# Optimization experiments

Hardware: AMD Instinct MI355X
Metric: run time of the kernel (lower is better)

Reference implementation:

```python
import jax, jax.numpy as jnp
import numpy as np

PAD = 50
CLUSTERING_WEIGHT = 1.0
SAMPLE_NUMBER = 8192
EPS = 1e-6


def setup_inputs() -> dict:
    key = jax.random.key(0)
    k1, k2 = jax.random.split(key)
    n, c, h, w = 2, 19, 512, 512
    output = jax.random.uniform(k1, (n, c, h, w), dtype=jnp.float32)
    hw_cropped = (h - 2 * PAD) * (w - 2 * PAD)  # 412*412 = 169744
    sample = jax.random.randint(k2, (SAMPLE_NUMBER,), 0, hw_cropped, dtype=jnp.int64)
    return {"output": output, "sample": sample}


def reference(output, sample):
    n, c, h, w = output.shape
    # crop pad border
    out = output[:, :, PAD:h - PAD, PAD:w - PAD]  # [n, c, h', w']
    prob = out.reshape(n, c, -1)[:, :, sample]     # [n, c, S]
    prob_t = jnp.swapaxes(prob, 1, 2)              # [n, S, c]
    # sampled similarity: [n, S, S] (memory-heavy intermediate)
    sim = jnp.einsum('nsc,ntc->nst', prob_t, prob_t)
    ind = jnp.argmax(sim, axis=2)                  # [n, S]
    # nearest[b, i, k] = prob_t[b, ind[b, i], k]
    nearest = jnp.take_along_axis(prob_t, ind[:, :, None], axis=1)  # [n, S, c]
    # robust_crossentropy(pred=prob_t, tgt=nearest)
    loss = -(nearest * jnp.log(prob_t + EPS))
    loss = loss.mean() * CLUSTERING_WEIGHT
    return loss[None]  # shape [1]
```

## Files before the change

kernel.cpp:

```cpp
#include <hip/hip_runtime.h>
#include <math.h>

#define N 2
#define C 19
#define H 512
#define W 512
#define PADC 50
#define WC 412
#define S 8192
#define CP 20
#define XP 64
#define NCHUNK 16
#define CHUNKT (S / NCHUNK)
#define TTS 128
#define NSTG (CHUNKT / TTS)
#define TPS (TTS / 32)
#define LPITCH 72
#define EPSF 1e-6f

typedef __attribute__((ext_vector_type(8))) short short8;
typedef __attribute__((ext_vector_type(16))) float f32x16;

__device__ __forceinline__ unsigned short f2bf_rne(float x) {
    unsigned u = __float_as_uint(x);
    unsigned r = (u + 0x7FFFu + ((u >> 16) & 1u)) >> 16;
    return (unsigned short)r;
}
__device__ __forceinline__ float bf2f(unsigned short h) {
    return __uint_as_float(((unsigned)h) << 16);
}
__device__ __forceinline__ float max16c(const f32x16 a) {
    float m0 = fmaxf(fmaxf(a[0], a[1]), a[2]);
    float m1 = fmaxf(fmaxf(a[3], a[4]), a[5]);
    float m2 = fmaxf(fmaxf(a[6], a[7]), a[8]);
    float m3 = fmaxf(fmaxf(a[9], a[10]), a[11]);
    float m4 = fmaxf(fmaxf(a[12], a[13]), a[14]);
    float n0 = fmaxf(fmaxf(m0, m1), m2);
    float n1 = fmaxf(fmaxf(m3, m4), a[15]);
    return fmaxf(fmaxf(n0, n1), 0.f);
}

__global__ void gather_k(const float* __restrict__ out4d,
                         const int* __restrict__ sample,
                         float* __restrict__ P32,
                         unsigned short* __restrict__ XA,
                         unsigned short* __restrict__ XB) {
    int idx = blockIdx.x * blockDim.x + threadIdx.x;
    int lane = idx & 63;
    int hi   = lane >> 5;
    int l    = lane & 31;
    int ns = idx >> 5;
    int nn = ns >> 13;
    int s  = ns & (S - 1);
    int smp = sample[s];
    int row = smp / WC;
    int col = smp - row * WC;
    const float* base = out4d + ((size_t)nn * C) * H * W
                      + (size_t)(PADC + row) * W + (PADC + col);
    float v = 0.f;
    if (l < C) v = base[(size_t)l * (H * W)];
    unsigned hb = f2bf_rne(v);
    unsigned lb = f2bf_rne(v - bf2f((unsigned short)hb));

    if (l < CP) P32[(size_t)ns * CP + l] = v;

    int base32 = hi << 5;
    int srcA = base32 + (l < C ? l : l - C);
    int srcB = base32 + (l < C ? l : l - 6);
    unsigned lbA = (unsigned)__shfl((int)lb, srcA, 64);
    unsigned hbA = (unsigned)__shfl((int)hb, srcA, 64);
    unsigned lbB = (unsigned)__shfl((int)lb, srcB, 64);
    unsigned hbB = (unsigned)__shfl((int)hb, srcB, 64);

    unsigned short a0 = (unsigned short)(l < C ? hb : lbA);
    unsigned short a1 = (unsigned short)(l < C ? hb : (l < 25 ? lbB : 0u));
    unsigned short b0 = (unsigned short)hbA;
    unsigned short b1 = (unsigned short)(l < C ? lb : (l < 25 ? hbB : 0u));

    unsigned short* xa = XA + (size_t)ns * XP;
    unsigned short* xb = XB + (size_t)ns * XP;
    xa[l]      = a0;
    xa[32 + l] = a1;
    xb[l]      = b0;
    xb[32 + l] = b1;
}

__global__ __launch_bounds__(512, 4) void argmax_k(const unsigned short* __restrict__ XA,
                                                   const unsigned short* __restrict__ XB,
                                                   unsigned* __restrict__ keys) {
    __shared__ unsigned short lds[2][TTS * LPITCH];
    int b = blockIdx.x;
    int chunk  = b & (NCHUNK - 1);
    int sgroup = (b >> 4) & 15;
    int nn     = b >> 8;
    int tid  = threadIdx.x;
    int w    = tid >> 6;
    int lane = tid & 63;
    int col  = lane & 31;
    int hi   = lane >> 5;
    int s0   = (sgroup * 16 + w) * 32;
    int s1   = s0 + 256;
    int t0   = chunk * CHUNKT;
    const unsigned short* XAn = XA + (size_t)nn * S * XP;
    const unsigned short* XBn = XB + (size_t)nn * S * XP;

    short8 bfA[4], bfB[4];
    {
        const unsigned short* ba = XBn + (size_t)(s0 + col) * XP + hi * 8;
        bfA[0] = *(const short8*)(ba);      bfA[1] = *(const short8*)(ba + 16);
        bfA[2] = *(const short8*)(ba + 32); bfA[3] = *(const short8*)(ba + 48);
        const unsigned short* bb = XBn + (size_t)(s1 + col) * XP + hi * 8;
        bfB[0] = *(const short8*)(bb);      bfB[1] = *(const short8*)(bb + 16);
        bfB[2] = *(const short8*)(bb + 32); bfB[3] = *(const short8*)(bb + 48);
    }

    f32x16 zacc = {};
    unsigned kA = 0u, kB = 0u;

    int r0 = tid >> 3, j0 = tid & 7;
    int r1 = r0 + 64;

    {
        const float4* src = (const float4*)(XAn + (size_t)t0 * XP);
        *(float4*)(&lds[0][r0 * LPITCH + j0 * 8]) = src[tid];
        *(float4*)(&lds[0][r1 * LPITCH + j0 * 8]) = src[tid + 512];
    }
    __syncthreads();

    int cur = 0;
    for (int st = 0; st < NSTG; ++st) {
        float4 na, nb;
        if (st + 1 < NSTG) {
            const float4* srcn = (const float4*)(XAn + (size_t)(t0 + (st + 1) * TTS) * XP);
            na = srcn[tid]; nb = srcn[tid + 512];
        }
        const unsigned short* bs = &lds[cur][0];
        #pragma unroll
        for (int ts = 0; ts < TPS; ++ts) {
            const unsigned short* arow = bs + (ts * 32 + col) * LPITCH + hi * 8;
            short8 a0 = *(const short8*)(arow);
            short8 a1 = *(const short8*)(arow + 16);
            short8 a2 = *(const short8*)(arow + 32);
            short8 a3 = *(const short8*)(arow + 48);
            f32x16 accA = __builtin_amdgcn_mfma_f32_32x32x16_bf16(a0, bfA[0], zacc, 0, 0, 0);
            accA = __builtin_amdgcn_mfma_f32_32x32x16_bf16(a1, bfA[1], accA, 0, 0, 0);
            accA = __builtin_amdgcn_mfma_f32_32x32x16_bf16(a2, bfA[2], accA, 0, 0, 0);
            accA = __builtin_amdgcn_mfma_f32_32x32x16_bf16(a3, bfA[3], accA, 0, 0, 0);
            f32x16 accB = __builtin_amdgcn_mfma_f32_32x32x16_bf16(a0, bfB[0], zacc, 0, 0, 0);
            accB = __builtin_amdgcn_mfma_f32_32x32x16_bf16(a1, bfB[1], accB, 0, 0, 0);
            accB = __builtin_amdgcn_mfma_f32_32x32x16_bf16(a2, bfB[2], accB, 0, 0, 0);
            accB = __builtin_amdgcn_mfma_f32_32x32x16_bf16(a3, bfB[3], accB, 0, 0, 0);
            int tile = st * TPS + ts;
            unsigned tb = (unsigned)(63 - tile);
            unsigned vA = (__float_as_uint(max16c(accA)) & ~63u) | tb;
            unsigned vB = (__float_as_uint(max16c(accB)) & ~63u) | tb;
            kA = kA > vA ? kA : vA;
            kB = kB > vB ? kB : vB;
        }
        if (st + 1 < NSTG) {
            *(float4*)(&lds[cur ^ 1][r0 * LPITCH + j0 * 8]) = na;
            *(float4*)(&lds[cur ^ 1][r1 * LPITCH + j0 * 8]) = nb;
        }
        __syncthreads();
        cur ^= 1;
    }

    unsigned oA = __shfl(kA, lane ^ 32, 64);
    unsigned oB = __shfl(kB, lane ^ 32, 64);
    kA = kA > oA ? kA : oA;
    kB = kB > oB ? kB : oB;
    if (lane < 32) {
        size_t basek = ((size_t)nn * NCHUNK + chunk) * S;
        keys[basek + s0 + col] = kA;
        keys[basek + s1 + col] = kB;
    }
}

__global__ __launch_bounds__(256) void refine_loss_k(const float* __restrict__ P32,
                                                     const unsigned* __restrict__ keys,
                                                     float* __restrict__ bsum) {
    __shared__ float red[8];
    int tid = threadIdx.x;
    int lane = tid & 63;
    int hi = lane >> 5;
    int l  = lane & 31;
    int ns = blockIdx.x * 8 + (tid >> 6) * 2 + hi;
    int nn = ns >> 13;
    int s  = ns & (S - 1);

    const unsigned* kp = keys + (size_t)nn * NCHUNK * S + s;
    unsigned bk = kp[0]; int bc = 0;
    #pragma unroll
    for (int c = 1; c < NCHUNK; ++c) {
        unsigned k = kp[(size_t)c * S];
        if ((k >> 6) > (bk >> 6)) { bk = k; bc = c; }
    }
    int tile = 63 - (int)(bk & 63u);
    int tbase = bc * CHUNKT + tile * 32;

    const float* Pn = P32 + (size_t)nn * S * CP;
    const float* sr = Pn + (size_t)s * CP;
    const float* tr = Pn + (size_t)(tbase + l) * CP;
    float v = 0.f;
    #pragma unroll
    for (int c = 0; c < C; ++c) v = fmaf(sr[c], tr[c], v);
    int t = tbase + l;
    #pragma unroll
    for (int off = 16; off > 0; off >>= 1) {
        float ov = __shfl_xor(v, off, 32);
        int   ot = __shfl_xor(t, off, 32);
        if (ov > v || (ov == v && ot < t)) { v = ov; t = ot; }
    }
    const float* nrow = Pn + (size_t)t * CP;
    float term = 0.f;
    if (l < C) term = -nrow[l] * logf(sr[l] + EPSF);
    #pragma unroll
    for (int off = 16; off > 0; off >>= 1)
        term += __shfl_xor(term, off, 32);
    if (l == 0) red[tid >> 5] = term;
    __syncthreads();
    if (tid == 0) {
        float a = 0.f;
        #pragma unroll
        for (int i = 0; i < 8; ++i) a += red[i];
        bsum[blockIdx.x] = a;
    }
}

__global__ __launch_bounds__(256) void final_k(const float* __restrict__ bsum,
                                               float* __restrict__ out) {
    __shared__ float red[256];
    int tid = threadIdx.x;
    float a = 0.f;
    #pragma unroll
    for (int i = 0; i < 8; ++i) a += bsum[i * 256 + tid];
    red[tid] = a;
    __syncthreads();
    for (int off = 128; off > 0; off >>= 1) {
        if (tid < off) red[tid] += red[tid + off];
        __syncthreads();
    }
    if (tid == 0) out[0] = red[0] / (float)(N * S * C);
}

extern "C" void kernel_launch(void* const* d_in, const int* in_sizes, int n_in,
                              void* d_out, int out_size, void* d_ws, size_t ws_size,
                              hipStream_t stream) {
    const float* out4d  = (const float*)d_in[0];
    const int*   sample = (const int*)d_in[1];

    float*          P32  = (float*)d_ws;
    unsigned short* XA   = (unsigned short*)(P32 + (size_t)N * S * CP);
    unsigned short* XB   = XA + (size_t)N * S * XP;
    unsigned*       keys = (unsigned*)(XB + (size_t)N * S * XP);
    float*          bsum = (float*)(keys + (size_t)N * NCHUNK * S);
    float*          outp = (float*)d_out;

    gather_k<<<(N * S * 32) / 256, 256, 0, stream>>>(out4d, sample, P32, XA, XB);
    argmax_k<<<N * 16 * NCHUNK, 512, 0, stream>>>(XA, XB, keys);
    refine_loss_k<<<(N * S) / 8, 256, 0, stream>>>(P32, keys, bsum);
    final_k<<<1, 256, 0, stream>>>(bsum, outp);
}
```

Baseline: 36.20 us.

## Give each argmax wave four B tiles and fuse final reduction via last-block atomic

```diff
diff --git a/kernel.cpp b/kernel.cpp
--- a/kernel.cpp
+++ b/kernel.cpp
@@ -16,6 +16,7 @@
 #define NSTG (CHUNKT / TTS)
 #define TPS (TTS / 32)
 #define LPITCH 72
+#define NBLK ((N * S) / 8)
 #define EPSF 1e-6f
 
 typedef __attribute__((ext_vector_type(8))) short short8;
@@ -44,8 +45,10 @@
                          const int* __restrict__ sample,
                          float* __restrict__ P32,
                          unsigned short* __restrict__ XA,
-                         unsigned short* __restrict__ XB) {
+                         unsigned short* __restrict__ XB,
+                         unsigned* __restrict__ counter) {
     int idx = blockIdx.x * blockDim.x + threadIdx.x;
+    if (idx == 0) counter[0] = 0u;
     int lane = idx & 63;
     int hi   = lane >> 5;
     int l    = lane & 31;
@@ -85,7 +88,7 @@
     xb[32 + l] = b1;
 }
 
-__global__ __launch_bounds__(512, 4) void argmax_k(const unsigned short* __restrict__ XA,
+__global__ __launch_bounds__(256, 3) void argmax_k(const unsigned short* __restrict__ XA,
                                                    const unsigned short* __restrict__ XB,
                                                    unsigned* __restrict__ keys) {
     __shared__ unsigned short lds[2][TTS * LPITCH];
@@ -98,41 +101,42 @@
     int lane = tid & 63;
     int col  = lane & 31;
     int hi   = lane >> 5;
-    int s0   = (sgroup * 16 + w) * 32;
-    int s1   = s0 + 256;
     int t0   = chunk * CHUNKT;
     const unsigned short* XAn = XA + (size_t)nn * S * XP;
     const unsigned short* XBn = XB + (size_t)nn * S * XP;
 
-    short8 bfA[4], bfB[4];
-    {
-        const unsigned short* ba = XBn + (size_t)(s0 + col) * XP + hi * 8;
-        bfA[0] = *(const short8*)(ba);      bfA[1] = *(const short8*)(ba + 16);
-        bfA[2] = *(const short8*)(ba + 32); bfA[3] = *(const short8*)(ba + 48);
-        const unsigned short* bb = XBn + (size_t)(s1 + col) * XP + hi * 8;
-        bfB[0] = *(const short8*)(bb);      bfB[1] = *(const short8*)(bb + 16);
-        bfB[2] = *(const short8*)(bb + 32); bfB[3] = *(const short8*)(bb + 48);
+    int sb[4];
+    short8 bf[4][4];
+    #pragma unroll
+    for (int j = 0; j < 4; ++j) {
+        sb[j] = sgroup * 512 + (w * 4 + j) * 32;
+        const unsigned short* bp = XBn + (size_t)(sb[j] + col) * XP + hi * 8;
+        bf[j][0] = *(const short8*)(bp);
+        bf[j][1] = *(const short8*)(bp + 16);
+        bf[j][2] = *(const short8*)(bp + 32);
+        bf[j][3] = *(const short8*)(bp + 48);
     }
 
     f32x16 zacc = {};
-    unsigned kA = 0u, kB = 0u;
-
-    int r0 = tid >> 3, j0 = tid & 7;
-    int r1 = r0 + 64;
+    unsigned key[4] = {0u, 0u, 0u, 0u};
 
     {
         const float4* src = (const float4*)(XAn + (size_t)t0 * XP);
-        *(float4*)(&lds[0][r0 * LPITCH + j0 * 8]) = src[tid];
-        *(float4*)(&lds[0][r1 * LPITCH + j0 * 8]) = src[tid + 512];
+        #pragma unroll
+        for (int k = 0; k < 4; ++k) {
+            int f = k * 256 + tid;
+            *(float4*)(&lds[0][(f >> 3) * LPITCH + (f & 7) * 8]) = src[f];
+        }
     }
     __syncthreads();
 
     int cur = 0;
     for (int st = 0; st < NSTG; ++st) {
-        float4 na, nb;
+        float4 nx[4];
         if (st + 1 < NSTG) {
             const float4* srcn = (const float4*)(XAn + (size_t)(t0 + (st + 1) * TTS) * XP);
-            na = srcn[tid]; nb = srcn[tid + 512];
+            #pragma unroll
+            for (int k = 0; k < 4; ++k) nx[k] = srcn[k * 256 + tid];
         }
         const unsigned short* bs = &lds[cur][0];
         #pragma unroll
@@ -142,44 +146,46 @@
             short8 a1 = *(const short8*)(arow + 16);
             short8 a2 = *(const short8*)(arow + 32);
             short8 a3 = *(const short8*)(arow + 48);
-            f32x16 accA = __builtin_amdgcn_mfma_f32_32x32x16_bf16(a0, bfA[0], zacc, 0, 0, 0);
-            accA = __builtin_amdgcn_mfma_f32_32x32x16_bf16(a1, bfA[1], accA, 0, 0, 0);
-            accA = __builtin_amdgcn_mfma_f32_32x32x16_bf16(a2, bfA[2], accA, 0, 0, 0);
-            accA = __builtin_amdgcn_mfma_f32_32x32x16_bf16(a3, bfA[3], accA, 0, 0, 0);
-            f32x16 accB = __builtin_amdgcn_mfma_f32_32x32x16_bf16(a0, bfB[0], zacc, 0, 0, 0);
-            accB = __builtin_amdgcn_mfma_f32_32x32x16_bf16(a1, bfB[1], accB, 0, 0, 0);
-            accB = __builtin_amdgcn_mfma_f32_32x32x16_bf16(a2, bfB[2], accB, 0, 0, 0);
-            accB = __builtin_amdgcn_mfma_f32_32x32x16_bf16(a3, bfB[3], accB, 0, 0, 0);
             int tile = st * TPS + ts;
             unsigned tb = (unsigned)(63 - tile);
-            unsigned vA = (__float_as_uint(max16c(accA)) & ~63u) | tb;
-            unsigned vB = (__float_as_uint(max16c(accB)) & ~63u) | tb;
-            kA = kA > vA ? kA : vA;
-            kB = kB > vB ? kB : vB;
+            #pragma unroll
+            for (int j = 0; j < 4; ++j) {
+                f32x16 acc = __builtin_amdgcn_mfma_f32_32x32x16_bf16(a0, bf[j][0], zacc, 0, 0, 0);
+                acc = __builtin_amdgcn_mfma_f32_32x32x16_bf16(a1, bf[j][1], acc, 0, 0, 0);
+                acc = __builtin_amdgcn_mfma_f32_32x32x16_bf16(a2, bf[j][2], acc, 0, 0, 0);
+                acc = __builtin_amdgcn_mfma_f32_32x32x16_bf16(a3, bf[j][3], acc, 0, 0, 0);
+                unsigned v = (__float_as_uint(max16c(acc)) & ~63u) | tb;
+                key[j] = key[j] > v ? key[j] : v;
+            }
         }
         if (st + 1 < NSTG) {
-            *(float4*)(&lds[cur ^ 1][r0 * LPITCH + j0 * 8]) = na;
-            *(float4*)(&lds[cur ^ 1][r1 * LPITCH + j0 * 8]) = nb;
+            #pragma unroll
+            for (int k = 0; k < 4; ++k) {
+                int f = k * 256 + tid;
+                *(float4*)(&lds[cur ^ 1][(f >> 3) * LPITCH + (f & 7) * 8]) = nx[k];
+            }
         }
         __syncthreads();
         cur ^= 1;
     }
 
-    unsigned oA = __shfl(kA, lane ^ 32, 64);
-    unsigned oB = __shfl(kB, lane ^ 32, 64);
-    kA = kA > oA ? kA : oA;
-    kB = kB > oB ? kB : oB;
-    if (lane < 32) {
-        size_t basek = ((size_t)nn * NCHUNK + chunk) * S;
-        keys[basek + s0 + col] = kA;
-        keys[basek + s1 + col] = kB;
+    size_t basek = ((size_t)nn * NCHUNK + chunk) * S;
+    #pragma unroll
+    for (int j = 0; j < 4; ++j) {
+        unsigned o = __shfl(key[j], lane ^ 32, 64);
+        unsigned k = key[j] > o ? key[j] : o;
+        if (lane < 32) keys[basek + sb[j] + col] = k;
     }
 }
 
 __global__ __launch_bounds__(256) void refine_loss_k(const float* __restrict__ P32,
                                                      const unsigned* __restrict__ keys,
-                                                     float* __restrict__ bsum) {
+                                                     float* __restrict__ bsum,
+                                                     unsigned* __restrict__ counter,
+                                                     float* __restrict__ out) {
     __shared__ float red[8];
+    __shared__ float fred[256];
+    __shared__ unsigned rank;
     int tid = threadIdx.x;
     int lane = tid & 63;
     int hi = lane >> 5;
@@ -224,23 +230,23 @@
         #pragma unroll
         for (int i = 0; i < 8; ++i) a += red[i];
         bsum[blockIdx.x] = a;
-    }
-}
-
-__global__ __launch_bounds__(256) void final_k(const float* __restrict__ bsum,
-                                               float* __restrict__ out) {
-    __shared__ float red[256];
-    int tid = threadIdx.x;
-    float a = 0.f;
-    #pragma unroll
-    for (int i = 0; i < 8; ++i) a += bsum[i * 256 + tid];
-    red[tid] = a;
+        __threadfence();
+        rank = atomicAdd(counter, 1u);
+    }
     __syncthreads();
-    for (int off = 128; off > 0; off >>= 1) {
-        if (tid < off) red[tid] += red[tid + off];
+    if (rank == NBLK - 1) {
+        float a = 0.f;
+        #pragma unroll
+        for (int i = 0; i < NBLK / 256; ++i)
+            a += atomicAdd(&bsum[i * 256 + tid], 0.f);
+        fred[tid] = a;
         __syncthreads();
-    }
-    if (tid == 0) out[0] = red[0] / (float)(N * S * C);
+        for (int off = 128; off > 0; off >>= 1) {
+            if (tid < off) fred[tid] += fred[tid + off];
+            __syncthreads();
+        }
+        if (tid == 0) out[0] = fred[0] / (float)(N * S * C);
+    }
 }
 
 extern "C" void kernel_launch(void* const* d_in, const int* in_sizes, int n_in,
@@ -254,10 +260,10 @@
     unsigned short* XB   = XA + (size_t)N * S * XP;
     unsigned*       keys = (unsigned*)(XB + (size_t)N * S * XP);
     float*          bsum = (float*)(keys + (size_t)N * NCHUNK * S);
+    unsigned*       ctr  = (unsigned*)(bsum + NBLK);
     float*          outp = (float*)d_out;
 
-    gather_k<<<(N * S * 32) / 256, 256, 0, stream>>>(out4d, sample, P32, XA, XB);
-    argmax_k<<<N * 16 * NCHUNK, 512, 0, stream>>>(XA, XB, keys);
-    refine_loss_k<<<(N * S) / 8, 256, 0, stream>>>(P32, keys, bsum);
-    final_k<<<1, 256, 0, stream>>>(bsum, outp);
-}
+    gather_k<<<(N * S * 32) / 256, 256, 0, stream>>>(out4d, sample, P32, XA, XB, ctr);
+    argmax_k<<<N * 16 * NCHUNK, 256, 0, stream>>>(XA, XB, keys);
+    refine_loss_k<<<NBLK, 256, 0, stream>>>(P32, keys, bsum, ctr, outp);
+}
```

After: 71.11 us. +96.4%, slower.
